# Kernel tuning notes

Measured on AMD Instinct MI355X. Metric: run time of the kernel, lower is better.

Reference implementation:

```python
import jax, jax.numpy as jnp
import numpy as np

NEG_SLOPE = 0.2  # PyG GATConv leaky_relu slope
EPS = 1e-16


def gat_layer(x, W, att_src, att_dst, bias, src, dst, num_nodes, heads, out_c, concat):
    # x: [N, F_in], W: [F_in, heads*out_c], att_*: [heads, out_c], bias: [heads*out_c] or [out_c]
    xp = (x @ W).reshape(num_nodes, heads, out_c)              # [N, H, C]
    a_src = (xp * att_src).sum(-1)                             # [N, H]
    a_dst = (xp * att_dst).sum(-1)                             # [N, H]
    alpha = jax.nn.leaky_relu(a_src[src] + a_dst[dst], NEG_SLOPE)  # [E, H]
    # segment softmax over destination-node neighborhoods
    m = jax.ops.segment_max(alpha, dst, num_segments=num_nodes)   # [N, H]
    e = jnp.exp(alpha - m[dst])
    s = jax.ops.segment_sum(e, dst, num_segments=num_nodes)
    alpha = e / (s[dst] + EPS)                                 # [E, H]
    out = jax.ops.segment_sum(xp[src] * alpha[:, :, None], dst, num_segments=num_nodes)  # [N, H, C]
    out = out.reshape(num_nodes, heads * out_c) if concat else out.mean(axis=1)
    return out + bias


def setup_inputs() -> dict:
    key = jax.random.key(0)
    N, E, F = 100000, 3200000, 128
    ks = jax.random.split(key, 10)
    x = jax.random.normal(ks[0], (N, F), dtype=jnp.float32)
    edge_index = jax.random.randint(ks[1], (2, E), 0, N, dtype=jnp.int64)
    s1 = 1.0 / np.sqrt(F)
    W1 = jax.random.normal(ks[2], (F, 2 * 16), dtype=jnp.float32) * s1
    att_src1 = jax.random.normal(ks[3], (2, 16), dtype=jnp.float32) * 0.25
    att_dst1 = jax.random.normal(ks[4], (2, 16), dtype=jnp.float32) * 0.25
    b1 = jnp.zeros((32,), dtype=jnp.float32)
    W2 = jax.random.normal(ks[5], (32, 1), dtype=jnp.float32) * (1.0 / np.sqrt(32))
    att_src2 = jax.random.normal(ks[6], (1, 1), dtype=jnp.float32)
    att_dst2 = jax.random.normal(ks[7], (1, 1), dtype=jnp.float32)
    b2 = jnp.zeros((1,), dtype=jnp.float32)
    return {"x": x, "edge_index": edge_index, "W1": W1, "att_src1": att_src1,
            "att_dst1": att_dst1, "b1": b1, "W2": W2, "att_src2": att_src2,
            "att_dst2": att_dst2, "b2": b2}


def reference(x, edge_index, W1, att_src1, att_dst1, b1, W2, att_src2, att_dst2, b2):
    N = x.shape[0]
    # PyG GATConv adds self-loops by default
    loops = jnp.arange(N, dtype=edge_index.dtype)
    src = jnp.concatenate([edge_index[0], loops])
    dst = jnp.concatenate([edge_index[1], loops])
    h = gat_layer(x, W1, att_src1, att_dst1, b1, src, dst, N, 2, 16, True)   # [N, 32]
    h = jax.nn.relu(h)
    out = gat_layer(h, W2, att_src2, att_dst2, b2, src, dst, N, 1, 1, False)  # [N, 1]
    return out.sum(axis=0, keepdims=True)  # [1, 1]
```

## Files before the change

### kernel.cpp

```cpp
#include <hip/hip_runtime.h>
#include <hip/hip_bf16.h>
#include <hip/hip_fp16.h>
#include <hip/hip_fp8.h>
#include <math.h>

#define NEG_SLOPE 0.2f
#define EPS 1e-16f
#define CHUNK 4096
#define BSH 8
#define BNODES 256

__device__ __forceinline__ float leaky(float x) {
    return x > 0.f ? x : NEG_SLOPE * x;
}

__global__ __launch_bounds__(1024) void chunkhist_kernel(
    const int* __restrict__ ei, int E, int ET, int NB, int NC,
    int* __restrict__ cnt) {
    __shared__ int histL[1024];
    int t = threadIdx.x;
    int c = blockIdx.x;
    if (t < NB) histL[t] = 0;
    __syncthreads();
    int e0 = c * CHUNK;
#pragma unroll 4
    for (int i = t; i < CHUNK; i += 1024) {
        int e = e0 + i;
        if (e < ET) {
            int d = (e < E) ? ei[E + e] : (e - E);
            atomicAdd(&histL[d >> BSH], 1);
        }
    }
    __syncthreads();
    if (t < NB) cnt[(size_t)t * NC + c] = histL[t];
}

__global__ void scan_block(const int* __restrict__ in, int* __restrict__ out,
                           int* __restrict__ partials, int n) {
    __shared__ int tmp[1024];
    int t = threadIdx.x;
    int g = blockIdx.x * 1024 + t;
    int v = (g < n) ? in[g] : 0;
    tmp[t] = v;
    __syncthreads();
    for (int off = 1; off < 1024; off <<= 1) {
        int add = (t >= off) ? tmp[t - off] : 0;
        __syncthreads();
        tmp[t] += add;
        __syncthreads();
    }
    if (g < n) out[g] = tmp[t] - v;
    if (t == 1023) partials[blockIdx.x] = tmp[1023];
}

__global__ void scan_partials(int* __restrict__ partials, int P) {
    __shared__ int tmp[1024];
    int t = threadIdx.x;
    int v = (t < P) ? partials[t] : 0;
    tmp[t] = v;
    __syncthreads();
    for (int off = 1; off < 1024; off <<= 1) {
        int add = (t >= off) ? tmp[t - off] : 0;
        __syncthreads();
        tmp[t] += add;
        __syncthreads();
    }
    if (t < P) partials[t] = tmp[t] - v;
}

__device__ __forceinline__ int gscan(const int* scanned, const int* partials,
                                     size_t g) {
    return scanned[g] + partials[g >> 10];
}

__global__ __launch_bounds__(1024) void packsort_kernel(
    const int* __restrict__ ei, int E, int ET, int NB, int NC,
    const int* __restrict__ scanned, const int* __restrict__ partials,
    unsigned int* __restrict__ packed) {
    __shared__ unsigned int sortedL[CHUNK];
    __shared__ int gposL[CHUNK];
    __shared__ int histL[1024];
    __shared__ int tmpL[1024];
    __shared__ int cursorL[1024];
    __shared__ int diffL[1024];
    int t = threadIdx.x;
    int c = blockIdx.x;
    int e0 = c * CHUNK;
    int cw = ET - e0; if (cw > CHUNK) cw = CHUNK;

    if (t < NB) histL[t] = 0;
    __syncthreads();

    unsigned int pk[4]; int bb[4];
#pragma unroll
    for (int k = 0; k < 4; k++) {
        int i = t + k * 1024;
        bb[k] = -1;
        if (i < cw) {
            int e = e0 + i;
            int s, d;
            if (e < E) { s = ei[e]; d = ei[E + e]; } else { s = d = e - E; }
            bb[k] = d >> BSH;
            pk[k] = ((unsigned int)s << BSH) | (unsigned int)(d & (BNODES - 1));
            atomicAdd(&histL[bb[k]], 1);
        }
    }
    __syncthreads();
    int hv = (t < NB) ? histL[t] : 0;
    tmpL[t] = hv;
    __syncthreads();
    for (int off = 1; off < 1024; off <<= 1) {
        int add = (t >= off) ? tmpL[t - off] : 0;
        __syncthreads();
        tmpL[t] += add;
        __syncthreads();
    }
    if (t < NB) {
        int loff = tmpL[t] - hv;
        cursorL[t] = loff;
        size_t g = (size_t)t * NC + c;
        diffL[t] = gscan(scanned, partials, g) - loff;
    }
    __syncthreads();
#pragma unroll
    for (int k = 0; k < 4; k++) {
        if (bb[k] >= 0) {
            int lpos = atomicAdd(&cursorL[bb[k]], 1);
            sortedL[lpos] = pk[k];
            gposL[lpos] = diffL[bb[k]] + lpos;
        }
    }
    __syncthreads();
    for (int i = t; i < cw; i += 1024)
        packed[gposL[i]] = sortedL[i];
}

__global__ __launch_bounds__(1024) void localsort_kernel(
    const unsigned int* __restrict__ packed, const int* __restrict__ scanned,
    const int* __restrict__ partials, int NB, int NC, int ET,
    int* __restrict__ srt, int* __restrict__ binptr, int N) {
    __shared__ int histL[BNODES];
    __shared__ int offL[BNODES];
    __shared__ int curL[BNODES];
    int t = threadIdx.x;
    int bkt = blockIdx.x;
    int base = bkt * BNODES;
    int ebeg = gscan(scanned, partials, (size_t)bkt * NC);
    int eend = (bkt + 1 < NB) ? gscan(scanned, partials, (size_t)(bkt + 1) * NC) : ET;
    if (t < BNODES) histL[t] = 0;
    __syncthreads();
    for (int i = ebeg + t; i < eend; i += 1024)
        atomicAdd(&histL[packed[i] & (BNODES - 1)], 1);
    __syncthreads();
    if (t < BNODES) offL[t] = histL[t];
    __syncthreads();
    for (int off = 1; off < BNODES; off <<= 1) {
        int add = (t >= off && t < BNODES) ? offL[t - off] : 0;
        __syncthreads();
        if (t < BNODES) offL[t] += add;
        __syncthreads();
    }
    if (t < BNODES) {
        int ex = offL[t] - histL[t];
        curL[t] = ex;
        int gn = base + t;
        if (gn < N) binptr[gn] = ebeg + ex;
    }
    if (bkt == 0 && t == 0) binptr[N] = ET;
    __syncthreads();
    for (int i = ebeg + t; i < eend; i += 1024) {
        unsigned int p = packed[i];
        int dl = p & (BNODES - 1);
        int pos = ebeg + atomicAdd(&curL[dl], 1);
        srt[pos] = (int)(p >> BSH);
    }
}

__global__ __launch_bounds__(256) void gemm1_kernel(
    const float* __restrict__ x, const float* __restrict__ W1,
    const float* __restrict__ att_src, const float* __restrict__ att_dst,
    __hip_fp8_e4m3* __restrict__ xp1f8, float* __restrict__ a_src,
    float* __restrict__ a_dst, int N) {
    __shared__ float wS[128 * 32];
    __shared__ float xS[8 * 128];
    int t = threadIdx.x;
    for (int i = t; i < 128 * 32 / 4; i += 256)
        ((float4*)wS)[i] = ((const float4*)W1)[i];
    int row0 = blockIdx.x * 8;
    int rmax = N - row0;
    int lr = t >> 5;
    if (lr < rmax)
        ((float4*)xS)[t] = ((const float4*)(x + (size_t)row0 * 128))[t];
    __syncthreads();

    int r = t >> 5, col = t & 31;
    int row = row0 + r;
    const float* xrow = xS + r * 128;
    float sum = 0.f;
#pragma unroll 8
    for (int k = 0; k < 128; k++)
        sum = fmaf(xrow[k], wS[k * 32 + col], sum);

    int h = col >> 4;
    float va = sum * att_src[col];
    float vd = sum * att_dst[col];
#pragma unroll
    for (int off = 8; off >= 1; off >>= 1) {
        va += __shfl_xor(va, off);
        vd += __shfl_xor(vd, off);
    }
    if (row < N) {
        xp1f8[(size_t)row * 32 + col] = __hip_fp8_e4m3(sum);
        if ((col & 15) == 0) {
            a_src[row * 2 + h] = va;
            a_dst[row * 2 + h] = vd;
        }
    }
}

__global__ __launch_bounds__(256) void agg1_kernel(
    const int* __restrict__ binptr, const int* __restrict__ srt,
    const float2* __restrict__ a_src2, const float2* __restrict__ a_dst2,
    const unsigned char* __restrict__ xp1f8, const float* __restrict__ b1,
    const float* __restrict__ W2, float* __restrict__ xp2, int N) {
    int tg = blockIdx.x * blockDim.x + threadIdx.x;
    int n = tg >> 6;
    int lane = threadIdx.x & 63;
    if (n >= N) return;
    int eg = lane >> 3;
    int cq = lane & 7;
    int hsel = cq >> 2;
    int beg = binptr[n], end = binptr[n + 1];
    float2 ad = a_dst2[n];
    const unsigned char* xpb = xp1f8 + cq * 4;

    float acc0 = 0.f, acc1 = 0.f, acc2 = 0.f, acc3 = 0.f, ssum = 0.f;
    for (int i0 = beg; i0 < end; i0 += 64) {
        int cw = end - i0;
        if (cw > 64) cw = 64;
        int s_l = 0;
        unsigned int pk_l = 0u;
        if (lane < cw) {
            s_l = srt[i0 + lane];
            float2 as = a_src2[s_l];
            float e0 = __expf(leaky(as.x + ad.x));
            float e1 = __expf(leaky(as.y + ad.y));
            pk_l = ((__float_as_uint(e1) + 0x8000u) & 0xFFFF0000u) |
                   ((__float_as_uint(e0) + 0x8000u) >> 16);
        }
#pragma unroll
        for (int k = 0; k < 8; k++) {
            int es = k * 8 + eg;
            int sk = __shfl(s_l, es);
            unsigned int pw = (unsigned int)__shfl((int)pk_l, es);
            float ek = __uint_as_float(hsel ? (pw & 0xFFFF0000u) : (pw << 16));
            unsigned int u = *(const unsigned int*)(xpb + (size_t)sk * 32);
            const __hip_fp8_e4m3* f4 = reinterpret_cast<const __hip_fp8_e4m3*>(&u);
            acc0 = fmaf(ek, (float)f4[0], acc0);
            acc1 = fmaf(ek, (float)f4[1], acc1);
            acc2 = fmaf(ek, (float)f4[2], acc2);
            acc3 = fmaf(ek, (float)f4[3], acc3);
            ssum += ek;
        }
    }
#pragma unroll
    for (int off = 8; off <= 32; off <<= 1) {
        acc0 += __shfl_xor(acc0, off);
        acc1 += __shfl_xor(acc1, off);
        acc2 += __shfl_xor(acc2, off);
        acc3 += __shfl_xor(acc3, off);
        ssum += __shfl_xor(ssum, off);
    }
    float inv = 1.f / (ssum + EPS);
    int j0 = cq * 4;
    float p;
    {
        float hv0 = fmaxf(acc0 * inv + b1[j0 + 0], 0.f);
        float hv1 = fmaxf(acc1 * inv + b1[j0 + 1], 0.f);
        float hv2 = fmaxf(acc2 * inv + b1[j0 + 2], 0.f);
        float hv3 = fmaxf(acc3 * inv + b1[j0 + 3], 0.f);
        p = hv0 * W2[j0 + 0];
        p = fmaf(hv1, W2[j0 + 1], p);
        p = fmaf(hv2, W2[j0 + 2], p);
        p = fmaf(hv3, W2[j0 + 3], p);
    }
    p += __shfl_xor(p, 1);
    p += __shfl_xor(p, 2);
    p += __shfl_xor(p, 4);
    if (lane == 0) xp2[n] = p;
}

__global__ __launch_bounds__(256) void agg2_kernel(
    const int* __restrict__ binptr, const int* __restrict__ srt,
    const float* __restrict__ xp2, const float* __restrict__ as2p,
    const float* __restrict__ ad2p, const float* __restrict__ b2,
    float* __restrict__ partial, int N) {
    int slot = (blockIdx.x * blockDim.x + threadIdx.x) >> 5;
    int j = threadIdx.x & 31;
    int nslots = (gridDim.x * blockDim.x) >> 5;
    float as2 = as2p[0], ad2 = ad2p[0], bb = b2[0];
    float val = 0.f;
    for (int n = slot; n < N; n += nslots) {
        int beg = binptr[n], end = binptr[n + 1];
        float xd = xp2[n] * ad2;
        float se = 0.f, sa = 0.f;
        for (int i = beg + j; i < end; i += 32) {
            float xs = xp2[srt[i]];
            float ex = __expf(leaky(fmaf(xs, as2, xd)));
            se += ex;
            sa = fmaf(ex, xs, sa);
        }
#pragma unroll
        for (int off = 16; off >= 1; off >>= 1) {
            se += __shfl_xor(se, off);
            sa += __shfl_xor(sa, off);
        }
        if (j == 0) val += sa / (se + EPS) + bb;
    }
#pragma unroll
    for (int off = 32; off >= 1; off >>= 1) val += __shfl_xor(val, off);
    __shared__ float ls[4];
    int lane = threadIdx.x & 63, w = threadIdx.x >> 6;
    if (lane == 0) ls[w] = val;
    __syncthreads();
    if (threadIdx.x == 0) partial[blockIdx.x] = ls[0] + ls[1] + ls[2] + ls[3];
}

__global__ void final_reduce(const float* __restrict__ partial, float* __restrict__ out,
                             int P) {
    int t = threadIdx.x;
    float v = 0.f;
    for (int i = t; i < P; i += 1024) v += partial[i];
#pragma unroll
    for (int off = 32; off >= 1; off >>= 1) v += __shfl_xor(v, off);
    __shared__ float ls[16];
    int w = t >> 6, lane = t & 63;
    if (lane == 0) ls[w] = v;
    __syncthreads();
    if (t == 0) {
        float s = 0.f;
        for (int i = 0; i < 16; i++) s += ls[i];
        out[0] = s;
    }
}

extern "C" void kernel_launch(void* const* d_in, const int* in_sizes, int n_in,
                              void* d_out, int out_size, void* d_ws, size_t ws_size,
                              hipStream_t stream) {
    const float* x        = (const float*)d_in[0];
    const int*   ei       = (const int*)d_in[1];
    const float* W1       = (const float*)d_in[2];
    const float* att_src1 = (const float*)d_in[3];
    const float* att_dst1 = (const float*)d_in[4];
    const float* b1       = (const float*)d_in[5];
    const float* W2       = (const float*)d_in[6];
    const float* att_src2 = (const float*)d_in[7];
    const float* att_dst2 = (const float*)d_in[8];
    const float* b2       = (const float*)d_in[9];
    float* out = (float*)d_out;

    int N = in_sizes[0] / 128;
    int E = in_sizes[1] / 2;
    int ET = E + N;
    int NB = (N + BNODES - 1) / BNODES;
    int NC = (ET + CHUNK - 1) / CHUNK;
    int n_scan = NB * NC;
    int nb2 = (n_scan + 1023) / 1024;
    const int AGG2_BLOCKS = 2048;

    char* w = (char*)d_ws;
    unsigned char* xp1f8 = (unsigned char*)w; w += (size_t)N * 32;
    float* a_src   = (float*)w;  w += sizeof(float) * (size_t)N * 2;
    float* a_dst   = (float*)w;  w += sizeof(float) * (size_t)N * 2;
    float* xp2     = (float*)w;  w += sizeof(float) * (size_t)N;
    int* cnt       = (int*)w;    w += sizeof(int) * (size_t)n_scan;
    int* scanned   = (int*)w;    w += sizeof(int) * (size_t)(n_scan + 4);
    int* partials  = (int*)w;    w += sizeof(int) * 1024;
    float* part2   = (float*)w;  w += sizeof(float) * (size_t)AGG2_BLOCKS;
    unsigned int* packed = (unsigned int*)w; w += sizeof(unsigned int) * (size_t)ET;
    int* srt       = (int*)w;    w += sizeof(int) * (size_t)ET;
    int* binptr    = (int*)w;    w += sizeof(int) * (size_t)(N + 1);

    gemm1_kernel<<<(N + 7) / 8, 256, 0, stream>>>(x, W1, att_src1, att_dst1,
                                                  (__hip_fp8_e4m3*)xp1f8, a_src,
                                                  a_dst, N);
    chunkhist_kernel<<<NC, 1024, 0, stream>>>(ei, E, ET, NB, NC, cnt);
    scan_block<<<nb2, 1024, 0, stream>>>(cnt, scanned, partials, n_scan);
    scan_partials<<<1, 1024, 0, stream>>>(partials, nb2);
    packsort_kernel<<<NC, 1024, 0, stream>>>(ei, E, ET, NB, NC, scanned, partials,
                                             packed);
    localsort_kernel<<<NB, 1024, 0, stream>>>(packed, scanned, partials, NB, NC, ET,
                                              srt, binptr, N);
    agg1_kernel<<<(N * 64 + 255) / 256, 256, 0, stream>>>(binptr, srt,
                                                          (const float2*)a_src,
                                                          (const float2*)a_dst,
                                                          xp1f8, b1, W2, xp2, N);
    agg2_kernel<<<AGG2_BLOCKS, 256, 0, stream>>>(binptr, srt, xp2,
                                                 att_src2, att_dst2, b2, part2, N);
    final_reduce<<<1, 1024, 0, stream>>>(part2, out, AGG2_BLOCKS);
}
```

Measured before the change: 174.3 us.

## Register-tile gemm1 over 64 rows and trim agg1 inner loop

```diff
diff --git a/kernel.cpp b/kernel.cpp
--- a/kernel.cpp
+++ b/kernel.cpp
@@ -176,44 +176,82 @@
     }
 }
 
+__device__ __forceinline__ void fma4(float4& acc, float sc, const float4& wv) {
+    acc.x = fmaf(sc, wv.x, acc.x);
+    acc.y = fmaf(sc, wv.y, acc.y);
+    acc.z = fmaf(sc, wv.z, acc.z);
+    acc.w = fmaf(sc, wv.w, acc.w);
+}
+
 __global__ __launch_bounds__(256) void gemm1_kernel(
     const float* __restrict__ x, const float* __restrict__ W1,
-    const float* __restrict__ att_src, const float* __restrict__ att_dst,
-    __hip_fp8_e4m3* __restrict__ xp1f8, float* __restrict__ a_src,
+    const float4* __restrict__ att_src4, const float4* __restrict__ att_dst4,
+    unsigned int* __restrict__ xp1u, float* __restrict__ a_src,
     float* __restrict__ a_dst, int N) {
-    __shared__ float wS[128 * 32];
-    __shared__ float xS[8 * 128];
-    int t = threadIdx.x;
-    for (int i = t; i < 128 * 32 / 4; i += 256)
-        ((float4*)wS)[i] = ((const float4*)W1)[i];
-    int row0 = blockIdx.x * 8;
-    int rmax = N - row0;
-    int lr = t >> 5;
-    if (lr < rmax)
-        ((float4*)xS)[t] = ((const float4*)(x + (size_t)row0 * 128))[t];
-    __syncthreads();
-
-    int r = t >> 5, col = t & 31;
-    int row = row0 + r;
-    const float* xrow = xS + r * 128;
-    float sum = 0.f;
-#pragma unroll 8
-    for (int k = 0; k < 128; k++)
-        sum = fmaf(xrow[k], wS[k * 32 + col], sum);
-
-    int h = col >> 4;
-    float va = sum * att_src[col];
-    float vd = sum * att_dst[col];
-#pragma unroll
-    for (int off = 8; off >= 1; off >>= 1) {
-        va += __shfl_xor(va, off);
-        vd += __shfl_xor(vd, off);
-    }
-    if (row < N) {
-        xp1f8[(size_t)row * 32 + col] = __hip_fp8_e4m3(sum);
-        if ((col & 15) == 0) {
-            a_src[row * 2 + h] = va;
-            a_dst[row * 2 + h] = vd;
+    __shared__ float4 wS4[128 * 8];
+    __shared__ float4 xS4[64 * 32];
+    int t = threadIdx.x;
+    int base = blockIdx.x * 64;
+#pragma unroll
+    for (int i = 0; i < 4; i++)
+        wS4[t + i * 256] = ((const float4*)W1)[t + i * 256];
+#pragma unroll
+    for (int i = 0; i < 8; i++) {
+        int idx = t + i * 256;
+        int row = idx >> 5, kb = idx & 31;
+        xS4[idx] = (base + row < N) ? ((const float4*)x)[(size_t)(base + row) * 32 + kb]
+                                    : make_float4(0.f, 0.f, 0.f, 0.f);
+    }
+    __syncthreads();
+
+    int cq = t & 7;
+    int rg = t >> 3;
+    const float4* xr0 = xS4 + (rg * 2) * 32;
+    const float4* xr1 = xr0 + 32;
+    float4 a0 = make_float4(0.f, 0.f, 0.f, 0.f);
+    float4 a1 = make_float4(0.f, 0.f, 0.f, 0.f);
+#pragma unroll 4
+    for (int kb = 0; kb < 32; kb++) {
+        float4 x0 = xr0[kb];
+        float4 x1 = xr1[kb];
+        float4 w0 = wS4[(kb * 4 + 0) * 8 + cq];
+        float4 w1 = wS4[(kb * 4 + 1) * 8 + cq];
+        float4 w2 = wS4[(kb * 4 + 2) * 8 + cq];
+        float4 w3 = wS4[(kb * 4 + 3) * 8 + cq];
+        fma4(a0, x0.x, w0); fma4(a0, x0.y, w1); fma4(a0, x0.z, w2); fma4(a0, x0.w, w3);
+        fma4(a1, x1.x, w0); fma4(a1, x1.y, w1); fma4(a1, x1.z, w2); fma4(a1, x1.w, w3);
+    }
+
+    float4 asv = att_src4[cq];
+    float4 adv = att_dst4[cq];
+    int r0 = base + rg * 2, r1 = r0 + 1;
+    float va0 = a0.x * asv.x + a0.y * asv.y + a0.z * asv.z + a0.w * asv.w;
+    float vd0 = a0.x * adv.x + a0.y * adv.y + a0.z * adv.z + a0.w * adv.w;
+    float va1 = a1.x * asv.x + a1.y * asv.y + a1.z * asv.z + a1.w * asv.w;
+    float vd1 = a1.x * adv.x + a1.y * adv.y + a1.z * adv.z + a1.w * adv.w;
+#pragma unroll
+    for (int off = 1; off <= 2; off <<= 1) {
+        va0 += __shfl_xor(va0, off);
+        vd0 += __shfl_xor(vd0, off);
+        va1 += __shfl_xor(va1, off);
+        vd1 += __shfl_xor(vd1, off);
+    }
+    if (r0 < N) {
+        __hip_fp8x4_e4m3 q0(a0);
+        xp1u[(size_t)r0 * 8 + cq] = *(unsigned int*)&q0;
+        if ((cq & 3) == 0) {
+            int h = cq >> 2;
+            a_src[r0 * 2 + h] = va0;
+            a_dst[r0 * 2 + h] = vd0;
+        }
+    }
+    if (r1 < N) {
+        __hip_fp8x4_e4m3 q1(a1);
+        xp1u[(size_t)r1 * 8 + cq] = *(unsigned int*)&q1;
+        if ((cq & 3) == 0) {
+            int h = cq >> 2;
+            a_src[r1 * 2 + h] = va1;
+            a_dst[r1 * 2 + h] = vd1;
         }
     }
 }
@@ -248,18 +286,19 @@
             pk_l = ((__float_as_uint(e1) + 0x8000u) & 0xFFFF0000u) |
                    ((__float_as_uint(e0) + 0x8000u) >> 16);
         }
-#pragma unroll
-        for (int k = 0; k < 8; k++) {
+        int kmax = (cw + 7) >> 3;
+#pragma unroll 2
+        for (int k = 0; k < kmax; k++) {
             int es = k * 8 + eg;
             int sk = __shfl(s_l, es);
             unsigned int pw = (unsigned int)__shfl((int)pk_l, es);
             float ek = __uint_as_float(hsel ? (pw & 0xFFFF0000u) : (pw << 16));
             unsigned int u = *(const unsigned int*)(xpb + (size_t)sk * 32);
-            const __hip_fp8_e4m3* f4 = reinterpret_cast<const __hip_fp8_e4m3*>(&u);
-            acc0 = fmaf(ek, (float)f4[0], acc0);
-            acc1 = fmaf(ek, (float)f4[1], acc1);
-            acc2 = fmaf(ek, (float)f4[2], acc2);
-            acc3 = fmaf(ek, (float)f4[3], acc3);
+            float4 xv = (float4)(*reinterpret_cast<const __hip_fp8x4_e4m3*>(&u));
+            acc0 = fmaf(ek, xv.x, acc0);
+            acc1 = fmaf(ek, xv.y, acc1);
+            acc2 = fmaf(ek, xv.z, acc2);
+            acc3 = fmaf(ek, xv.w, acc3);
             ssum += ek;
         }
     }
@@ -381,9 +420,11 @@
     int* srt       = (int*)w;    w += sizeof(int) * (size_t)ET;
     int* binptr    = (int*)w;    w += sizeof(int) * (size_t)(N + 1);
 
-    gemm1_kernel<<<(N + 7) / 8, 256, 0, stream>>>(x, W1, att_src1, att_dst1,
-                                                  (__hip_fp8_e4m3*)xp1f8, a_src,
-                                                  a_dst, N);
+    gemm1_kernel<<<(N + 63) / 64, 256, 0, stream>>>(x, W1,
+                                                    (const float4*)att_src1,
+                                                    (const float4*)att_dst1,
+                                                    (unsigned int*)xp1f8, a_src,
+                                                    a_dst, N);
     chunkhist_kernel<<<NC, 1024, 0, stream>>>(ei, E, ET, NB, NC, cnt);
     scan_block<<<nb2, 1024, 0, stream>>>(cnt, scanned, partials, n_scan);
     scan_partials<<<1, 1024, 0, stream>>>(partials, nb2);
```

Result: faster. 164.1 us (-5.8%).
